# Kernel tuning notes

Measured on AMD Instinct MI355X. Metric: run time of the kernel, lower is better.

The kernel has to match this reference:

```python
import jax, jax.numpy as jnp
import numpy as np

EPS = 1e-5

def ln(x, g, b):
    m = x.mean(-1, keepdims=True)
    v = x.var(-1, keepdims=True)
    return (x - m) / jnp.sqrt(v + EPS) * g + b

def setup_inputs() -> dict:
    key = jax.random.key(0)
    ks = jax.random.split(key, 16)
    def p(k, shape, fan):
        return jax.random.normal(k, shape, jnp.float32) * (1.0 / np.sqrt(fan))
    B, N, M = 4, 256, 256
    C = 256
    inp = {}
    inp["tracks"] = jax.random.normal(ks[0], (B, 1028, N), jnp.float32)
    inp["detections"] = jax.random.normal(ks[1], (B, 1028, M), jnp.float32)
    # app encoder: Linear(1024,256) -> LN -> ReLU -> Linear(256,256)
    inp["wa1"] = p(ks[2], (1024, C), 1024); inp["ba1"] = jnp.zeros((C,), jnp.float32)
    inp["gla"] = jnp.ones((C,), jnp.float32); inp["bla"] = jnp.zeros((C,), jnp.float32)
    inp["wa2"] = p(ks[3], (C, C), C); inp["ba2"] = jnp.zeros((C,), jnp.float32)
    # geo encoder: Linear(4,128) -> LN -> ReLU -> Linear(128,256)
    inp["wg1"] = p(ks[4], (4, C // 2), 4); inp["bg1"] = jnp.zeros((C // 2,), jnp.float32)
    inp["glg"] = jnp.ones((C // 2,), jnp.float32); inp["blg"] = jnp.zeros((C // 2,), jnp.float32)
    inp["wg2"] = p(ks[5], (C // 2, C), C // 2); inp["bg2"] = jnp.zeros((C,), jnp.float32)
    # fusion LayerNorm
    inp["gf"] = jnp.ones((C,), jnp.float32); inp["bf"] = jnp.zeros((C,), jnp.float32)
    # cross-attention (4 heads, head_dim 64)
    inp["wq"] = p(ks[6], (C, C), C); inp["bq"] = jnp.zeros((C,), jnp.float32)
    inp["wk"] = p(ks[7], (C, C), C); inp["bk"] = jnp.zeros((C,), jnp.float32)
    inp["wv"] = p(ks[8], (C, C), C); inp["bv"] = jnp.zeros((C,), jnp.float32)
    inp["wo"] = p(ks[9], (C, C), C); inp["bo"] = jnp.zeros((C,), jnp.float32)
    # classifier: Linear(512,128) -> ReLU -> Linear(128,1)
    inp["wc1"] = p(ks[10], (2 * C, 128), 2 * C); inp["bc1"] = jnp.zeros((128,), jnp.float32)
    inp["wc2"] = p(ks[11], (128, 1), 128); inp["bc2"] = jnp.zeros((1,), jnp.float32)
    return inp

def reference(tracks, detections, wa1, ba1, gla, bla, wa2, ba2,
              wg1, bg1, glg, blg, wg2, bg2, gf, bf,
              wq, bq, wk, bk, wv, bv, wo, bo,
              wc1, bc1, wc2, bc2):
    tr = tracks.transpose(0, 2, 1)       # (B, N, 1028)
    de = detections.transpose(0, 2, 1)   # (B, M, 1028)

    def encode(x):
        app, geo = x[..., :1024], x[..., 1024:]
        h = jax.nn.relu(ln(app @ wa1 + ba1, gla, bla)) @ wa2 + ba2
        g = jax.nn.relu(ln(geo @ wg1 + bg1, glg, blg)) @ wg2 + bg2
        return ln(h + g, gf, bf)

    t_emb = encode(tr)   # (B, N, C)
    d_emb = encode(de)   # (B, M, C)

    B, N, C = t_emb.shape
    M = d_emb.shape[1]
    H, dh = 4, C // 4

    # Cross-attention (computed in the original forward but its output is never used)
    q = (t_emb @ wq + bq).reshape(B, N, H, dh)
    k = (d_emb @ wk + bk).reshape(B, M, H, dh)
    v = (d_emb @ wv + bv).reshape(B, M, H, dh)
    att = jax.nn.softmax(jnp.einsum('bnhd,bmhd->bhnm', q, k) / jnp.sqrt(jnp.float32(dh)), axis=-1)
    attn_out = jnp.einsum('bhnm,bmhd->bnhd', att, v).reshape(B, N, C) @ wo + bo  # unused, as in original

    # Pairwise classifier. cat([t_rep, d_rep], -1) @ wc1 == t @ wc1[:C] + d @ wc1[C:]
    a = t_emb @ wc1[:C]   # (B, N, 128)
    c = d_emb @ wc1[C:]   # (B, M, 128)
    h = jax.nn.relu(a[:, :, None, :] + c[:, None, :, :] + bc1)  # (B, N, M, 128)
    logits = (h @ wc2 + bc2)[..., 0]  # (B, N, M)
    return logits
```

## Files before the change

kernel.cpp:

```cpp
#include <hip/hip_runtime.h>

#define EPS 1e-5f


__global__ __launch_bounds__(256) void k_gemm1(
    const float* __restrict__ tracks, const float* __restrict__ dets,
    const float* __restrict__ wa1, float* __restrict__ part)
{
    __shared__ float xs[128 * 20];
    const int blk = blockIdx.x;
    const int rt  = blk >> 3;
    const int ksi = blk & 7;
    const int g0  = rt * 16;
    const int side = g0 >> 10, b = (g0 >> 8) & 3, n0 = g0 & 255;
    const float* xb = (side ? dets : tracks) + (size_t)b * (1028 * 256);
    const int k0 = ksi * 128;
    const int c  = threadIdx.x;

    for (int idx = threadIdx.x; idx < 2048; idx += 256) {
        int f = idx >> 4, r = idx & 15;
        xs[f * 20 + r] = xb[(size_t)(k0 + f) * 256 + n0 + r];
    }
    __syncthreads();

    float acc[16];
#pragma unroll
    for (int i = 0; i < 16; ++i) acc[i] = 0.f;

#pragma unroll 2
    for (int f = 0; f < 128; ++f) {
        const float4* xr = (const float4*)(xs + f * 20);
        float4 v0 = xr[0], v1 = xr[1], v2 = xr[2], v3 = xr[3];
        float w = wa1[(size_t)(k0 + f) * 256 + c];
        acc[0]  = fmaf(v0.x, w, acc[0]);  acc[1]  = fmaf(v0.y, w, acc[1]);
        acc[2]  = fmaf(v0.z, w, acc[2]);  acc[3]  = fmaf(v0.w, w, acc[3]);
        acc[4]  = fmaf(v1.x, w, acc[4]);  acc[5]  = fmaf(v1.y, w, acc[5]);
        acc[6]  = fmaf(v1.z, w, acc[6]);  acc[7]  = fmaf(v1.w, w, acc[7]);
        acc[8]  = fmaf(v2.x, w, acc[8]);  acc[9]  = fmaf(v2.y, w, acc[9]);
        acc[10] = fmaf(v2.z, w, acc[10]); acc[11] = fmaf(v2.w, w, acc[11]);
        acc[12] = fmaf(v3.x, w, acc[12]); acc[13] = fmaf(v3.y, w, acc[13]);
        acc[14] = fmaf(v3.z, w, acc[14]); acc[15] = fmaf(v3.w, w, acc[15]);
    }
    float* pb = part + ((size_t)ksi * 2048 + g0) * 256 + c;
#pragma unroll
    for (int i = 0; i < 16; ++i) pb[(size_t)i * 256] = acc[i];
}

__global__ __launch_bounds__(256) void k_reduce1(
    const float* __restrict__ tracks, const float* __restrict__ dets,
    const float* __restrict__ part,
    const float* __restrict__ ba1, const float* __restrict__ gla,
    const float* __restrict__ bla,
    const float* __restrict__ wg1, const float* __restrict__ bg1,
    const float* __restrict__ glg, const float* __restrict__ blg,
    float* __restrict__ h1ext)
{
    __shared__ float red[4][4][2];
    __shared__ float geo_s[4][4];
    const int blk = blockIdx.x;
    const int g0 = blk * 4;
    const int side = g0 >> 10, b = (g0 >> 8) & 3, n0 = g0 & 255;
    const float* xb = (side ? dets : tracks) + (size_t)b * (1028 * 256);
    const int tid = threadIdx.x, wave = tid >> 6, lane = tid & 63, c = tid;

    if (tid < 16)
        geo_s[tid >> 2][tid & 3] =
            xb[(size_t)(1024 + (tid & 3)) * 256 + n0 + (tid >> 2)];

    float h[4];
#pragma unroll
    for (int i = 0; i < 4; ++i) {
        float s = ba1[c];
#pragma unroll
        for (int s8 = 0; s8 < 8; ++s8)
            s += part[((size_t)s8 * 2048 + g0 + i) * 256 + c];
        h[i] = s;
    }
#pragma unroll
    for (int i = 0; i < 4; ++i) {
        float s = h[i], s2 = h[i] * h[i];
#pragma unroll
        for (int off = 32; off >= 1; off >>= 1) {
            s  += __shfl_xor(s,  off, 64);
            s2 += __shfl_xor(s2, off, 64);
        }
        if (lane == 0) { red[wave][i][0] = s; red[wave][i][1] = s2; }
    }
    __syncthreads();
    {
        float gv = gla[c], bv = bla[c];
#pragma unroll
        for (int i = 0; i < 4; ++i) {
            float s  = red[0][i][0] + red[1][i][0] + red[2][i][0] + red[3][i][0];
            float s2 = red[0][i][1] + red[1][i][1] + red[2][i][1] + red[3][i][1];
            float m   = s * (1.f / 256.f);
            float var = s2 * (1.f / 256.f) - m * m;
            h1ext[(size_t)(g0 + i) * 384 + c] =
                fmaxf((h[i] - m) * rsqrtf(var + EPS) * gv + bv, 0.f);
        }
    }
    __syncthreads();

    float gh[4];
    if (tid < 128) {
        const int j = tid;
#pragma unroll
        for (int i = 0; i < 4; ++i) {
            float s = bg1[j];
#pragma unroll
            for (int f = 0; f < 4; ++f)
                s = fmaf(geo_s[i][f], wg1[f * 128 + j], s);
            gh[i] = s;
        }
#pragma unroll
        for (int i = 0; i < 4; ++i) {
            float s = gh[i], s2 = gh[i] * gh[i];
#pragma unroll
            for (int off = 32; off >= 1; off >>= 1) {
                s  += __shfl_xor(s,  off, 64);
                s2 += __shfl_xor(s2, off, 64);
            }
            if (lane == 0) { red[wave][i][0] = s; red[wave][i][1] = s2; }
        }
    }
    __syncthreads();
    if (tid < 128) {
        const int j = tid;
        float gv = glg[j], bv = blg[j];
#pragma unroll
        for (int i = 0; i < 4; ++i) {
            float s  = red[0][i][0] + red[1][i][0];
            float s2 = red[0][i][1] + red[1][i][1];
            float m   = s * (1.f / 128.f);
            float var = s2 * (1.f / 128.f) - m * m;
            h1ext[(size_t)(g0 + i) * 384 + 256 + j] =
                fmaxf((gh[i] - m) * rsqrtf(var + EPS) * gv + bv, 0.f);
        }
    }
}

__global__ __launch_bounds__(256) void k_gemm2(
    const float* __restrict__ h1ext,
    const float* __restrict__ wa2, const float* __restrict__ wg2,
    float* __restrict__ part)
{
    __shared__ float xs[64 * 20];
    const int blk = blockIdx.x;
    const int rt = blk / 6, sl = blk - rt * 6;
    const int g0 = rt * 16;
    const int k0 = sl * 64;
    const int c  = threadIdx.x;
    const float* Wb = (k0 < 256) ? (wa2 + (size_t)k0 * 256)
                                 : (wg2 + (size_t)(k0 - 256) * 256);

    for (int idx = threadIdx.x; idx < 1024; idx += 256) {
        int f = idx & 63, r = idx >> 6;
        xs[f * 20 + r] = h1ext[(size_t)(g0 + r) * 384 + k0 + f];
    }
    __syncthreads();

    float acc[16];
#pragma unroll
    for (int i = 0; i < 16; ++i) acc[i] = 0.f;

#pragma unroll 2
    for (int f = 0; f < 64; ++f) {
        const float4* xr = (const float4*)(xs + f * 20);
        float4 v0 = xr[0], v1 = xr[1], v2 = xr[2], v3 = xr[3];
        float w = Wb[(size_t)f * 256 + c];
        acc[0]  = fmaf(v0.x, w, acc[0]);  acc[1]  = fmaf(v0.y, w, acc[1]);
        acc[2]  = fmaf(v0.z, w, acc[2]);  acc[3]  = fmaf(v0.w, w, acc[3]);
        acc[4]  = fmaf(v1.x, w, acc[4]);  acc[5]  = fmaf(v1.y, w, acc[5]);
        acc[6]  = fmaf(v1.z, w, acc[6]);  acc[7]  = fmaf(v1.w, w, acc[7]);
        acc[8]  = fmaf(v2.x, w, acc[8]);  acc[9]  = fmaf(v2.y, w, acc[9]);
        acc[10] = fmaf(v2.z, w, acc[10]); acc[11] = fmaf(v2.w, w, acc[11]);
        acc[12] = fmaf(v3.x, w, acc[12]); acc[13] = fmaf(v3.y, w, acc[13]);
        acc[14] = fmaf(v3.z, w, acc[14]); acc[15] = fmaf(v3.w, w, acc[15]);
    }
    float* pb = part + ((size_t)sl * 2048 + g0) * 256 + c;
#pragma unroll
    for (int i = 0; i < 16; ++i) pb[(size_t)i * 256] = acc[i];
}

__global__ __launch_bounds__(256) void k_reduce2(
    const float* __restrict__ part,
    const float* __restrict__ ba2, const float* __restrict__ bg2,
    const float* __restrict__ gf,  const float* __restrict__ bf,
    const float* __restrict__ wc1,
    float* __restrict__ aout, float* __restrict__ cout)
{
    __shared__ float red[4][4][2];
    __shared__ float emb[256 * 4];
    __shared__ float psum[2][4][128];
    const int blk = blockIdx.x;
    const int g0 = blk * 4;
    const int side = g0 >> 10, b = (g0 >> 8) & 3, nin = g0 & 255;
    const int tid = threadIdx.x, wave = tid >> 6, lane = tid & 63, c = tid;

    float h2[4];
#pragma unroll
    for (int i = 0; i < 4; ++i) {
        float s = ba2[c] + bg2[c];
#pragma unroll
        for (int sl = 0; sl < 6; ++sl)
            s += part[((size_t)sl * 2048 + g0 + i) * 256 + c];
        h2[i] = s;
    }
#pragma unroll
    for (int i = 0; i < 4; ++i) {
        float s = h2[i], s2 = h2[i] * h2[i];
#pragma unroll
        for (int off = 32; off >= 1; off >>= 1) {
            s  += __shfl_xor(s,  off, 64);
            s2 += __shfl_xor(s2, off, 64);
        }
        if (lane == 0) { red[wave][i][0] = s; red[wave][i][1] = s2; }
    }
    __syncthreads();
    {
        float gv = gf[c], bv = bf[c];
        float e[4];
#pragma unroll
        for (int i = 0; i < 4; ++i) {
            float s  = red[0][i][0] + red[1][i][0] + red[2][i][0] + red[3][i][0];
            float s2 = red[0][i][1] + red[1][i][1] + red[2][i][1] + red[3][i][1];
            float m   = s * (1.f / 256.f);
            float var = s2 * (1.f / 256.f) - m * m;
            e[i] = (h2[i] - m) * rsqrtf(var + EPS) * gv + bv;
        }
        *(float4*)(emb + (size_t)c * 4) = make_float4(e[0], e[1], e[2], e[3]);
    }
    __syncthreads();

    const int half = tid >> 7, j = tid & 127;
    const float* wch = wc1 + (size_t)side * (256 * 128);
    float a4[4] = {0.f, 0.f, 0.f, 0.f};
#pragma unroll 4
    for (int k = 0; k < 128; ++k) {
        int kk = half * 128 + k;
        float w = wch[(size_t)kk * 128 + j];
        float4 ev = *(const float4*)(emb + kk * 4);
        a4[0] = fmaf(ev.x, w, a4[0]); a4[1] = fmaf(ev.y, w, a4[1]);
        a4[2] = fmaf(ev.z, w, a4[2]); a4[3] = fmaf(ev.w, w, a4[3]);
    }
#pragma unroll
    for (int i = 0; i < 4; ++i) psum[half][i][j] = a4[i];
    __syncthreads();

    float* outp = (side ? cout : aout) + ((size_t)b * 256 + nin) * 128;
    for (int idx = tid; idx < 512; idx += 256) {
        int i = idx >> 7, jo = idx & 127;
        outp[(size_t)i * 128 + jo] = psum[0][i][jo] + psum[1][i][jo];
    }
}

__global__ __launch_bounds__(256) void k_pairwise(
    const float* __restrict__ a, const float* __restrict__ cmat,
    const float* __restrict__ bc1, const float* __restrict__ wc2,
    const float* __restrict__ bc2, float* __restrict__ out)
{
    __shared__ float4 a_s[16 * 33];
    __shared__ float4 c_s[16 * 33];
    const int blk = blockIdx.x;
    const int b  = blk >> 8;
    const int n0 = ((blk >> 4) & 15) << 4;
    const int m0 = (blk & 15) << 4;
    const int tid = threadIdx.x;

    const float4* a4  = (const float4*)(a    + ((size_t)b * 256 + n0) * 128);
    const float4* c4  = (const float4*)(cmat + ((size_t)b * 256 + m0) * 128);
    const float4* b14 = (const float4*)bc1;
    for (int idx = tid; idx < 512; idx += 256) {
        int r = idx >> 5, q = idx & 31;
        float4 av = a4[r * 32 + q], bv = b14[q];
        a_s[r * 33 + q] = make_float4(av.x + bv.x, av.y + bv.y,
                                      av.z + bv.z, av.w + bv.w);
        c_s[r * 33 + q] = c4[r * 32 + q];
    }
    __syncthreads();

    const int ni = tid >> 4, mi = tid & 15;
    const float4* wp = (const float4*)wc2;
    float acc = bc2[0];
#pragma unroll 8
    for (int q = 0; q < 32; ++q) {
        float4 av = a_s[ni * 33 + q];
        float4 cv = c_s[mi * 33 + q];
        float4 wv = wp[q];
        acc = fmaf(fmaxf(av.x + cv.x, 0.f), wv.x, acc);
        acc = fmaf(fmaxf(av.y + cv.y, 0.f), wv.y, acc);
        acc = fmaf(fmaxf(av.z + cv.z, 0.f), wv.z, acc);
        acc = fmaf(fmaxf(av.w + cv.w, 0.f), wv.w, acc);
    }
    out[((size_t)b * 256 + n0 + ni) * 256 + m0 + mi] = acc;
}

extern "C" void kernel_launch(void* const* d_in, const int* in_sizes, int n_in,
                              void* d_out, int out_size, void* d_ws, size_t ws_size,
                              hipStream_t stream)
{
    const float* tracks = (const float*)d_in[0];
    const float* dets   = (const float*)d_in[1];
    const float* wa1 = (const float*)d_in[2];
    const float* ba1 = (const float*)d_in[3];
    const float* gla = (const float*)d_in[4];
    const float* bla = (const float*)d_in[5];
    const float* wa2 = (const float*)d_in[6];
    const float* ba2 = (const float*)d_in[7];
    const float* wg1 = (const float*)d_in[8];
    const float* bg1 = (const float*)d_in[9];
    const float* glg = (const float*)d_in[10];
    const float* blg = (const float*)d_in[11];
    const float* wg2 = (const float*)d_in[12];
    const float* bg2 = (const float*)d_in[13];
    const float* gf  = (const float*)d_in[14];
    const float* bf  = (const float*)d_in[15];
    const float* wc1 = (const float*)d_in[24];
    const float* bc1 = (const float*)d_in[25];
    const float* wc2 = (const float*)d_in[26];
    const float* bc2 = (const float*)d_in[27];
    float* out = (float*)d_out;
    float* ws  = (float*)d_ws;

    float* part  = ws;
    float* h1ext = ws + 4194304;
    float* aa    = ws + 4980736;
    float* cc    = ws + 5111808;

    hipLaunchKernelGGL(k_gemm1, dim3(1024), dim3(256), 0, stream,
                       tracks, dets, wa1, part);
    hipLaunchKernelGGL(k_reduce1, dim3(512), dim3(256), 0, stream,
                       tracks, dets, part, ba1, gla, bla,
                       wg1, bg1, glg, blg, h1ext);
    hipLaunchKernelGGL(k_gemm2, dim3(768), dim3(256), 0, stream,
                       h1ext, wa2, wg2, part);
    hipLaunchKernelGGL(k_reduce2, dim3(512), dim3(256), 0, stream,
                       part, ba2, bg2, gf, bf, wc1, aa, cc);
    hipLaunchKernelGGL(k_pairwise, dim3(1024), dim3(256), 0, stream,
                       aa, cc, bc1, wc2, bc2, out);
}
```

Before: 176.4 us.

## Use 4x4 register tiles in GEMMs and 2x2 outputs per thread in pairwise

The two split-K GEMM kernels now give each thread a 4-row by 4-column register tile, using float4 weight loads and float4 stores, instead of 16 rows by 1 column. This cuts the LDS reads per FMA and vectorizes global weight traffic. The pairwise kernel now tiles 32x32 outputs per block, with each thread computing a 2x2 block, so a/c values loaded from LDS are reused across outputs. The pairwise launch drops to 256 blocks, which lowers occupancy across the GPU's CUs.

```diff
diff --git a/kernel.cpp b/kernel.cpp
--- a/kernel.cpp
+++ b/kernel.cpp
@@ -7,7 +7,7 @@
     const float* __restrict__ tracks, const float* __restrict__ dets,
     const float* __restrict__ wa1, float* __restrict__ part)
 {
-    __shared__ float xs[128 * 20];
+    __shared__ float xs[128 * 16];
     const int blk = blockIdx.x;
     const int rt  = blk >> 3;
     const int ksi = blk & 7;
@@ -15,35 +15,48 @@
     const int side = g0 >> 10, b = (g0 >> 8) & 3, n0 = g0 & 255;
     const float* xb = (side ? dets : tracks) + (size_t)b * (1028 * 256);
     const int k0 = ksi * 128;
-    const int c  = threadIdx.x;
-
-    for (int idx = threadIdx.x; idx < 2048; idx += 256) {
+    const int tid = threadIdx.x;
+    const int w   = tid >> 6;
+    const int c0  = (tid & 63) * 4;
+
+    for (int idx = tid; idx < 2048; idx += 256) {
         int f = idx >> 4, r = idx & 15;
-        xs[f * 20 + r] = xb[(size_t)(k0 + f) * 256 + n0 + r];
-    }
-    __syncthreads();
-
-    float acc[16];
-#pragma unroll
-    for (int i = 0; i < 16; ++i) acc[i] = 0.f;
+        xs[f * 16 + r] = xb[(size_t)(k0 + f) * 256 + n0 + r];
+    }
+    __syncthreads();
+
+    float acc[4][4];
+#pragma unroll
+    for (int i = 0; i < 4; ++i)
+#pragma unroll
+        for (int j = 0; j < 4; ++j) acc[i][j] = 0.f;
 
 #pragma unroll 2
     for (int f = 0; f < 128; ++f) {
-        const float4* xr = (const float4*)(xs + f * 20);
-        float4 v0 = xr[0], v1 = xr[1], v2 = xr[2], v3 = xr[3];
-        float w = wa1[(size_t)(k0 + f) * 256 + c];
-        acc[0]  = fmaf(v0.x, w, acc[0]);  acc[1]  = fmaf(v0.y, w, acc[1]);
-        acc[2]  = fmaf(v0.z, w, acc[2]);  acc[3]  = fmaf(v0.w, w, acc[3]);
-        acc[4]  = fmaf(v1.x, w, acc[4]);  acc[5]  = fmaf(v1.y, w, acc[5]);
-        acc[6]  = fmaf(v1.z, w, acc[6]);  acc[7]  = fmaf(v1.w, w, acc[7]);
-        acc[8]  = fmaf(v2.x, w, acc[8]);  acc[9]  = fmaf(v2.y, w, acc[9]);
-        acc[10] = fmaf(v2.z, w, acc[10]); acc[11] = fmaf(v2.w, w, acc[11]);
-        acc[12] = fmaf(v3.x, w, acc[12]); acc[13] = fmaf(v3.y, w, acc[13]);
-        acc[14] = fmaf(v3.z, w, acc[14]); acc[15] = fmaf(v3.w, w, acc[15]);
-    }
-    float* pb = part + ((size_t)ksi * 2048 + g0) * 256 + c;
-#pragma unroll
-    for (int i = 0; i < 16; ++i) pb[(size_t)i * 256] = acc[i];
+        float4 xv = *(const float4*)(xs + f * 16 + w * 4);
+        float4 wv = *(const float4*)(wa1 + (size_t)(k0 + f) * 256 + c0);
+        acc[0][0] = fmaf(xv.x, wv.x, acc[0][0]);
+        acc[0][1] = fmaf(xv.x, wv.y, acc[0][1]);
+        acc[0][2] = fmaf(xv.x, wv.z, acc[0][2]);
+        acc[0][3] = fmaf(xv.x, wv.w, acc[0][3]);
+        acc[1][0] = fmaf(xv.y, wv.x, acc[1][0]);
+        acc[1][1] = fmaf(xv.y, wv.y, acc[1][1]);
+        acc[1][2] = fmaf(xv.y, wv.z, acc[1][2]);
+        acc[1][3] = fmaf(xv.y, wv.w, acc[1][3]);
+        acc[2][0] = fmaf(xv.z, wv.x, acc[2][0]);
+        acc[2][1] = fmaf(xv.z, wv.y, acc[2][1]);
+        acc[2][2] = fmaf(xv.z, wv.z, acc[2][2]);
+        acc[2][3] = fmaf(xv.z, wv.w, acc[2][3]);
+        acc[3][0] = fmaf(xv.w, wv.x, acc[3][0]);
+        acc[3][1] = fmaf(xv.w, wv.y, acc[3][1]);
+        acc[3][2] = fmaf(xv.w, wv.z, acc[3][2]);
+        acc[3][3] = fmaf(xv.w, wv.w, acc[3][3]);
+    }
+    float* pb = part + ((size_t)ksi * 2048 + g0 + w * 4) * 256 + c0;
+#pragma unroll
+    for (int i = 0; i < 4; ++i)
+        *(float4*)(pb + (size_t)i * 256) =
+            make_float4(acc[i][0], acc[i][1], acc[i][2], acc[i][3]);
 }
 
 __global__ __launch_bounds__(256) void k_reduce1(
@@ -144,42 +157,55 @@
     const float* __restrict__ wa2, const float* __restrict__ wg2,
     float* __restrict__ part)
 {
-    __shared__ float xs[64 * 20];
+    __shared__ float xs[64 * 16];
     const int blk = blockIdx.x;
     const int rt = blk / 6, sl = blk - rt * 6;
     const int g0 = rt * 16;
     const int k0 = sl * 64;
-    const int c  = threadIdx.x;
+    const int tid = threadIdx.x;
+    const int w   = tid >> 6;
+    const int c0  = (tid & 63) * 4;
     const float* Wb = (k0 < 256) ? (wa2 + (size_t)k0 * 256)
                                  : (wg2 + (size_t)(k0 - 256) * 256);
 
-    for (int idx = threadIdx.x; idx < 1024; idx += 256) {
-        int f = idx & 63, r = idx >> 6;
-        xs[f * 20 + r] = h1ext[(size_t)(g0 + r) * 384 + k0 + f];
-    }
-    __syncthreads();
-
-    float acc[16];
-#pragma unroll
-    for (int i = 0; i < 16; ++i) acc[i] = 0.f;
+    for (int idx = tid; idx < 1024; idx += 256) {
+        int f = idx >> 4, r = idx & 15;
+        xs[f * 16 + r] = h1ext[(size_t)(g0 + r) * 384 + k0 + f];
+    }
+    __syncthreads();
+
+    float acc[4][4];
+#pragma unroll
+    for (int i = 0; i < 4; ++i)
+#pragma unroll
+        for (int j = 0; j < 4; ++j) acc[i][j] = 0.f;
 
 #pragma unroll 2
     for (int f = 0; f < 64; ++f) {
-        const float4* xr = (const float4*)(xs + f * 20);
-        float4 v0 = xr[0], v1 = xr[1], v2 = xr[2], v3 = xr[3];
-        float w = Wb[(size_t)f * 256 + c];
-        acc[0]  = fmaf(v0.x, w, acc[0]);  acc[1]  = fmaf(v0.y, w, acc[1]);
-        acc[2]  = fmaf(v0.z, w, acc[2]);  acc[3]  = fmaf(v0.w, w, acc[3]);
-        acc[4]  = fmaf(v1.x, w, acc[4]);  acc[5]  = fmaf(v1.y, w, acc[5]);
-        acc[6]  = fmaf(v1.z, w, acc[6]);  acc[7]  = fmaf(v1.w, w, acc[7]);
-        acc[8]  = fmaf(v2.x, w, acc[8]);  acc[9]  = fmaf(v2.y, w, acc[9]);
-        acc[10] = fmaf(v2.z, w, acc[10]); acc[11] = fmaf(v2.w, w, acc[11]);
-        acc[12] = fmaf(v3.x, w, acc[12]); acc[13] = fmaf(v3.y, w, acc[13]);
-        acc[14] = fmaf(v3.z, w, acc[14]); acc[15] = fmaf(v3.w, w, acc[15]);
-    }
-    float* pb = part + ((size_t)sl * 2048 + g0) * 256 + c;
-#pragma unroll
-    for (int i = 0; i < 16; ++i) pb[(size_t)i * 256] = acc[i];
+        float4 xv = *(const float4*)(xs + f * 16 + w * 4);
+        float4 wv = *(const float4*)(Wb + (size_t)f * 256 + c0);
+        acc[0][0] = fmaf(xv.x, wv.x, acc[0][0]);
+        acc[0][1] = fmaf(xv.x, wv.y, acc[0][1]);
+        acc[0][2] = fmaf(xv.x, wv.z, acc[0][2]);
+        acc[0][3] = fmaf(xv.x, wv.w, acc[0][3]);
+        acc[1][0] = fmaf(xv.y, wv.x, acc[1][0]);
+        acc[1][1] = fmaf(xv.y, wv.y, acc[1][1]);
+        acc[1][2] = fmaf(xv.y, wv.z, acc[1][2]);
+        acc[1][3] = fmaf(xv.y, wv.w, acc[1][3]);
+        acc[2][0] = fmaf(xv.z, wv.x, acc[2][0]);
+        acc[2][1] = fmaf(xv.z, wv.y, acc[2][1]);
+        acc[2][2] = fmaf(xv.z, wv.z, acc[2][2]);
+        acc[2][3] = fmaf(xv.z, wv.w, acc[2][3]);
+        acc[3][0] = fmaf(xv.w, wv.x, acc[3][0]);
+        acc[3][1] = fmaf(xv.w, wv.y, acc[3][1]);
+        acc[3][2] = fmaf(xv.w, wv.z, acc[3][2]);
+        acc[3][3] = fmaf(xv.w, wv.w, acc[3][3]);
+    }
+    float* pb = part + ((size_t)sl * 2048 + g0 + w * 4) * 256 + c0;
+#pragma unroll
+    for (int i = 0; i < 4; ++i)
+        *(float4*)(pb + (size_t)i * 256) =
+            make_float4(acc[i][0], acc[i][1], acc[i][2], acc[i][3]);
 }
 
 __global__ __launch_bounds__(256) void k_reduce2(
@@ -259,18 +285,18 @@
     const float* __restrict__ bc1, const float* __restrict__ wc2,
     const float* __restrict__ bc2, float* __restrict__ out)
 {
-    __shared__ float4 a_s[16 * 33];
-    __shared__ float4 c_s[16 * 33];
-    const int blk = blockIdx.x;
-    const int b  = blk >> 8;
-    const int n0 = ((blk >> 4) & 15) << 4;
-    const int m0 = (blk & 15) << 4;
+    __shared__ float4 a_s[32 * 33];
+    __shared__ float4 c_s[32 * 33];
+    const int blk = blockIdx.x;
+    const int b  = blk >> 6;
+    const int n0 = ((blk >> 3) & 7) << 5;
+    const int m0 = (blk & 7) << 5;
     const int tid = threadIdx.x;
 
     const float4* a4  = (const float4*)(a    + ((size_t)b * 256 + n0) * 128);
     const float4* c4  = (const float4*)(cmat + ((size_t)b * 256 + m0) * 128);
     const float4* b14 = (const float4*)bc1;
-    for (int idx = tid; idx < 512; idx += 256) {
+    for (int idx = tid; idx < 1024; idx += 256) {
         int r = idx >> 5, q = idx & 31;
         float4 av = a4[r * 32 + q], bv = b14[q];
         a_s[r * 33 + q] = make_float4(av.x + bv.x, av.y + bv.y,
@@ -281,18 +307,37 @@
 
     const int ni = tid >> 4, mi = tid & 15;
     const float4* wp = (const float4*)wc2;
-    float acc = bc2[0];
-#pragma unroll 8
+    float s00 = 0.f, s01 = 0.f, s10 = 0.f, s11 = 0.f;
+#pragma unroll 4
     for (int q = 0; q < 32; ++q) {
-        float4 av = a_s[ni * 33 + q];
-        float4 cv = c_s[mi * 33 + q];
-        float4 wv = wp[q];
-        acc = fmaf(fmaxf(av.x + cv.x, 0.f), wv.x, acc);
-        acc = fmaf(fmaxf(av.y + cv.y, 0.f), wv.y, acc);
-        acc = fmaf(fmaxf(av.z + cv.z, 0.f), wv.z, acc);
-        acc = fmaf(fmaxf(av.w + cv.w, 0.f), wv.w, acc);
-    }
-    out[((size_t)b * 256 + n0 + ni) * 256 + m0 + mi] = acc;
+        float4 av0 = a_s[ni * 33 + q];
+        float4 av1 = a_s[(ni + 16) * 33 + q];
+        float4 cv0 = c_s[mi * 33 + q];
+        float4 cv1 = c_s[(mi + 16) * 33 + q];
+        float4 wv  = wp[q];
+        s00 = fmaf(fmaxf(av0.x + cv0.x, 0.f), wv.x, s00);
+        s00 = fmaf(fmaxf(av0.y + cv0.y, 0.f), wv.y, s00);
+        s00 = fmaf(fmaxf(av0.z + cv0.z, 0.f), wv.z, s00);
+        s00 = fmaf(fmaxf(av0.w + cv0.w, 0.f), wv.w, s00);
+        s01 = fmaf(fmaxf(av0.x + cv1.x, 0.f), wv.x, s01);
+        s01 = fmaf(fmaxf(av0.y + cv1.y, 0.f), wv.y, s01);
+        s01 = fmaf(fmaxf(av0.z + cv1.z, 0.f), wv.z, s01);
+        s01 = fmaf(fmaxf(av0.w + cv1.w, 0.f), wv.w, s01);
+        s10 = fmaf(fmaxf(av1.x + cv0.x, 0.f), wv.x, s10);
+        s10 = fmaf(fmaxf(av1.y + cv0.y, 0.f), wv.y, s10);
+        s10 = fmaf(fmaxf(av1.z + cv0.z, 0.f), wv.z, s10);
+        s10 = fmaf(fmaxf(av1.w + cv0.w, 0.f), wv.w, s10);
+        s11 = fmaf(fmaxf(av1.x + cv1.x, 0.f), wv.x, s11);
+        s11 = fmaf(fmaxf(av1.y + cv1.y, 0.f), wv.y, s11);
+        s11 = fmaf(fmaxf(av1.z + cv1.z, 0.f), wv.z, s11);
+        s11 = fmaf(fmaxf(av1.w + cv1.w, 0.f), wv.w, s11);
+    }
+    const float b2 = bc2[0];
+    float* ob = out + ((size_t)b * 256 + n0) * 256 + m0;
+    ob[(size_t)ni * 256 + mi]               = s00 + b2;
+    ob[(size_t)ni * 256 + mi + 16]          = s01 + b2;
+    ob[(size_t)(ni + 16) * 256 + mi]        = s10 + b2;
+    ob[(size_t)(ni + 16) * 256 + mi + 16]   = s11 + b2;
 }
 
 extern "C" void kernel_launch(void* const* d_in, const int* in_sizes, int n_in,
@@ -336,6 +381,6 @@
                        h1ext, wa2, wg2, part);
     hipLaunchKernelGGL(k_reduce2, dim3(512), dim3(256), 0, stream,
                        part, ba2, bg2, gf, bf, wc1, aa, cc);
-    hipLaunchKernelGGL(k_pairwise, dim3(1024), dim3(256), 0, stream,
+    hipLaunchKernelGGL(k_pairwise, dim3(256), dim3(256), 0, stream,
                        aa, cc, bc1, wc2, bc2, out);
 }
```

Measured after the change: 177.7 us. Within noise of the previous version (+0.8%).
